# Kernel optimization log

Measured on AMD Instinct MI355X. Metric: run time of the kernel, lower is better.

Reference implementation:

```python
import jax, jax.numpy as jnp
import numpy as np

B = 4096
D = 2048
K = 8          # num_intention
H2 = 64        # fc2 out


def setup_inputs() -> dict:
    key = jax.random.key(0)
    ks = jax.random.split(key, 8)
    x = jax.random.normal(ks[0], (B, D), dtype=jnp.float32)
    # one-hot intention per sample
    idx = jax.random.randint(ks[1], (B,), 0, K)
    intention = jax.nn.one_hot(idx, K, dtype=jnp.float32)
    s1 = 1.0 / np.sqrt(D)
    s2 = 1.0 / np.sqrt(K)
    s3 = 1.0 / np.sqrt(D + H2)
    W1 = jax.random.uniform(ks[2], (D * K, D), jnp.float32, -s1, s1)
    b1 = jax.random.uniform(ks[3], (D * K,), jnp.float32, -s1, s1)
    W2 = jax.random.uniform(ks[4], (H2, K), jnp.float32, -s2, s2)
    b2 = jax.random.uniform(ks[5], (H2,), jnp.float32, -s2, s2)
    W3 = jax.random.uniform(ks[6], (1, D + H2), jnp.float32, -s3, s3)
    b3 = jax.random.uniform(ks[7], (1,), jnp.float32, -s3, s3)
    return {"x": x, "intention": intention, "W1": W1, "b1": b1,
            "W2": W2, "b2": b2, "W3": W3, "b3": b3}


def reference(x, intention, W1, b1, W2, b2, W3, b3):
    # fc2 on the one-hot intention -> [B, 64]
    y2 = intention @ W2.T + b2
    # fc1 densely computes all K branches (dropout treated as identity / eval mode)
    y1 = x @ W1.T + b1                      # [B, D*K]
    # mask = intention.repeat(1, 2048): branch axis is INNERMOST (interleaved)
    y1 = y1.reshape(B, D, K)                # [B, D, K]
    sel = jax.lax.stop_gradient(intention)  # mask is non-differentiable in torch
    y1 = jnp.einsum('bdk,bk->bd', y1, sel)  # gather active branch -> [B, D]
    y3 = jax.nn.relu(jnp.concatenate([y1, y2], axis=1))  # [B, D+64]
    y = y3 @ W3.T + b3                      # [B, 1]
    return y
```

## Files before the change

### kernel.cpp

```cpp
#include <hip/hip_runtime.h>
#include <hip/hip_bf16.h>
#include <stdint.h>

#define NB 4096
#define ND 2048
#define NK 8
#define NH 64

#define BM 128
#define BN 128
#define BK 32
#define MAX_ROWS 5120
#define MAX_TILES 40

#define CONV_BLOCKS  2048
#define KIDX_BLOCKS  (NB / 256)
#define PREP_GRID    (CONV_BLOCKS + KIDX_BLOCKS)
#define STRIPE 8388608

typedef __bf16 bf16;
typedef __bf16 bf16x8 __attribute__((ext_vector_type(8)));
typedef float floatx4 __attribute__((ext_vector_type(4)));

#define OFF_KIDX   0u
#define OFF_ORDER  16384u
#define OFF_META   40960u
#define OFF_CUR    41472u
#define OFF_C2S    41536u
#define OFF_CNTP   41600u
#define OFF_XC     65536u
#define OFF_WB     16842752u

__device__ inline void cvt16nt(const float* __restrict__ src, bf16* __restrict__ dst) {
    floatx4 a = __builtin_nontemporal_load((const floatx4*)src);
    floatx4 b = __builtin_nontemporal_load((const floatx4*)src + 1);
    floatx4 c = __builtin_nontemporal_load((const floatx4*)src + 2);
    floatx4 d = __builtin_nontemporal_load((const floatx4*)src + 3);
    bf16x8 v0, v1;
    v0[0] = (bf16)a[0]; v0[1] = (bf16)a[1]; v0[2] = (bf16)a[2]; v0[3] = (bf16)a[3];
    v0[4] = (bf16)b[0]; v0[5] = (bf16)b[1]; v0[6] = (bf16)b[2]; v0[7] = (bf16)b[3];
    v1[0] = (bf16)c[0]; v1[1] = (bf16)c[1]; v1[2] = (bf16)c[2]; v1[3] = (bf16)c[3];
    v1[4] = (bf16)d[0]; v1[5] = (bf16)d[1]; v1[6] = (bf16)d[2]; v1[7] = (bf16)d[3];
    *(bf16x8*)dst = v0;
    *((bf16x8*)dst + 1) = v1;
}

__global__ void __launch_bounds__(256)
prep_conv_kernel(const float* __restrict__ x,
                 const float* __restrict__ intention,
                 const float* __restrict__ W1,
                 int* __restrict__ kidx,
                 int* __restrict__ cntp,
                 bf16* __restrict__ xc,
                 bf16* __restrict__ Wb)
{
    const int blk = blockIdx.x;
    const int tid = threadIdx.x;

    if (blk < CONV_BLOCKS) {
        const size_t t16 = ((size_t)blk * 256 + tid) * 16;
#pragma unroll
        for (int i = 0; i < 4; i++)
            cvt16nt(W1 + (size_t)i * STRIPE + t16, Wb + (size_t)i * STRIPE + t16);
        cvt16nt(x + t16, xc + t16);
    } else {
        __shared__ int h[NK];
        const int hb = blk - CONV_BLOCKS;
        if (tid < NK) h[tid] = 0;
        __syncthreads();
        const int b = hb * 256 + tid;
        float4 a = *(const float4*)(intention + (size_t)b * NK);
        float4 c = *(const float4*)(intention + (size_t)b * NK + 4);
        int k = 0;
        if (a.y > 0.5f) k = 1;
        if (a.z > 0.5f) k = 2;
        if (a.w > 0.5f) k = 3;
        if (c.x > 0.5f) k = 4;
        if (c.y > 0.5f) k = 5;
        if (c.z > 0.5f) k = 6;
        if (c.w > 0.5f) k = 7;
        kidx[b] = k;
        atomicAdd(&h[k], 1);
        __syncthreads();
        if (tid < NK) cntp[hb * NK + tid] = h[tid];
    }
}

__global__ void __launch_bounds__(256)
meta_kernel(const int* __restrict__ cntp,
            const float* __restrict__ W2,
            const float* __restrict__ b2,
            const float* __restrict__ W3,
            const float* __restrict__ b3,
            int* __restrict__ meta,
            int* __restrict__ cursors,
            float* __restrict__ c2s)
{
    __shared__ int cnt[NK];
    const int tid = threadIdx.x;
    if (tid < NK) {
        int s = 0;
#pragma unroll
        for (int i = 0; i < KIDX_BLOCKS; i++) s += cntp[i * NK + tid];
        cnt[tid] = s;
    }
    if (tid >= 64 && tid < 128) {
        const int l = tid - 64;
        const int k = l & 7;
        const int hc = l >> 3;
        float s = 0.f;
#pragma unroll
        for (int j = 0; j < 8; j++) {
            int h = hc * 8 + j;
            float v = W2[h * NK + k] + b2[h];
            if (v > 0.f) s += v * W3[ND + h];
        }
        s += __shfl_xor(s, 8, 64);
        s += __shfl_xor(s, 16, 64);
        s += __shfl_xor(s, 32, 64);
        if (l < 8) c2s[k] = s + b3[0];
    }
    __syncthreads();
    if (tid == 0) {
        int running = 0, nt = 0;
        for (int k = 0; k < NK; k++) {
            cursors[k] = running;
            int ntile = (cnt[k] + BM - 1) / BM;
            for (int t = 0; t < ntile && nt < MAX_TILES; t++) {
                meta[1 + nt] = k;
                meta[1 + MAX_TILES + nt] = running + t * BM;
                nt++;
            }
            running += ntile * BM;
        }
        meta[0] = nt;
    }
}

__global__ void __launch_bounds__(256)
scatter_kernel(const int* __restrict__ kidx,
               int* __restrict__ cursors,
               const float* __restrict__ c2s,
               int* __restrict__ order,
               float* __restrict__ out)
{
    const int b = blockIdx.x * 256 + threadIdx.x;
    const int lane = threadIdx.x & 63;
    const int k = kidx[b] & 7;
    out[b] = c2s[k];

    const unsigned long long below = (lane == 63) ? ~0ull >> 1
                                   : ((1ull << lane) - 1);
    int pos = 0;
#pragma unroll
    for (int kk = 0; kk < NK; kk++) {
        unsigned long long m = __ballot(k == kk);
        if (m) {
            int leader = __ffsll((long long)m) - 1;
            int base = 0;
            if (lane == leader) base = atomicAdd(&cursors[kk], __popcll(m));
            base = __shfl(base, leader, 64);
            if (k == kk) pos = base + __popcll(m & below);
        }
    }
    if (pos >= 0 && pos < MAX_ROWS) order[pos] = b;
}

__global__ void __launch_bounds__(256)
gemm_kernel(const bf16* __restrict__ xc,
            const bf16* __restrict__ Wb,
            const int* __restrict__ order,
            const int* __restrict__ meta,
            const float* __restrict__ b1,
            const float* __restrict__ W3,
            float* __restrict__ out)
{
    int n_mt = meta[0];
    if (n_mt > MAX_TILES) n_mt = MAX_TILES;
    const int mt = blockIdx.y;
    if (mt >= n_mt) return;
    const int kbr = meta[1 + mt] & 7;
    int row0 = meta[1 + MAX_TILES + mt];
    if (row0 < 0) row0 = 0;
    if (row0 > MAX_ROWS - BM) row0 = MAX_ROWS - BM;
    const int col0 = blockIdx.x * BN;

    __shared__ bf16 As[BM * BK];
    __shared__ bf16 Bs[BN * BK];
    __shared__ int rowb[BM];

    const int tid = threadIdx.x;
    const int lane = tid & 63;
    const int wid = tid >> 6;
    const int wm = wid >> 1;
    const int wn = wid & 1;

    if (tid < BM) {
        int b = order[row0 + tid];
        rowb[tid] = (b >= 0 && b < NB) ? b : -1;
    }
    __syncthreads();

    const int srow = tid >> 2;
    const int scol = (tid & 3) * 8;
    const int ra0 = rowb[srow];
    const int ra1 = rowb[64 + srow];
    const bf16* pa0 = xc + (size_t)(ra0 < 0 ? 0 : ra0) * ND + scol;
    const bf16* pa1 = xc + (size_t)(ra1 < 0 ? 0 : ra1) * ND + scol;
    const bf16* pb0 = Wb + ((size_t)(col0 + srow) * NK + kbr) * ND + scol;
    const bf16* pb1 = pb0 + (size_t)64 * NK * ND;
    bf16* la0 = As + wid * 512;
    bf16* la1 = As + 2048 + wid * 512;
    bf16* lb0 = Bs + wid * 512;
    bf16* lb1 = Bs + 2048 + wid * 512;

    floatx4 zero = {0.f, 0.f, 0.f, 0.f};
    floatx4 acc[4][4];
#pragma unroll
    for (int i = 0; i < 4; i++)
#pragma unroll
        for (int j = 0; j < 4; j++) acc[i][j] = zero;

    const int qk = (lane >> 4) * 8;
    const int mrow = lane & 15;

    for (int kk = 0; kk < ND; kk += BK) {
        __builtin_amdgcn_global_load_lds(
            (const __attribute__((address_space(1))) void*)(pa0 + kk),
            (__attribute__((address_space(3))) void*)la0, 16, 0, 0);
        __builtin_amdgcn_global_load_lds(
            (const __attribute__((address_space(1))) void*)(pa1 + kk),
            (__attribute__((address_space(3))) void*)la1, 16, 0, 0);
        __builtin_amdgcn_global_load_lds(
            (const __attribute__((address_space(1))) void*)(pb0 + kk),
            (__attribute__((address_space(3))) void*)lb0, 16, 0, 0);
        __builtin_amdgcn_global_load_lds(
            (const __attribute__((address_space(1))) void*)(pb1 + kk),
            (__attribute__((address_space(3))) void*)lb1, 16, 0, 0);
        __syncthreads();

        bf16x8 af[4], bfv[4];
#pragma unroll
        for (int i = 0; i < 4; i++) {
            af[i]  = *(const bf16x8*)(As + (wm * 64 + i * 16 + mrow) * BK + qk);
            bfv[i] = *(const bf16x8*)(Bs + (wn * 64 + i * 16 + mrow) * BK + qk);
        }
#pragma unroll
        for (int i = 0; i < 4; i++)
#pragma unroll
            for (int j = 0; j < 4; j++)
                acc[i][j] = __builtin_amdgcn_mfma_f32_16x16x32_bf16(
                    af[i], bfv[j], acc[i][j], 0, 0, 0);
        __syncthreads();
    }

    const int colq = lane & 15;
    const int quad = lane >> 4;
    float bias[4], w3v[4];
#pragma unroll
    for (int j = 0; j < 4; j++) {
        int d = col0 + wn * 64 + j * 16 + colq;
        bias[j] = b1[d * NK + kbr];
        w3v[j] = W3[d];
    }
#pragma unroll
    for (int i = 0; i < 4; i++) {
#pragma unroll
        for (int r = 0; r < 4; r++) {
            float s = 0.f;
#pragma unroll
            for (int j = 0; j < 4; j++) {
                float v = acc[i][j][r] + bias[j];
                s += (v > 0.f) ? v * w3v[j] : 0.f;
            }
#pragma unroll
            for (int m = 1; m < 16; m <<= 1) s += __shfl_xor(s, m, 64);
            if (colq == 0) {
                int b = rowb[wm * 64 + i * 16 + quad * 4 + r];
                if (b >= 0) atomicAdd(out + b, s);
            }
        }
    }
}

extern "C" void kernel_launch(void* const* d_in, const int* in_sizes, int n_in,
                              void* d_out, int out_size, void* d_ws, size_t ws_size,
                              hipStream_t stream)
{
    const float* x         = (const float*)d_in[0];
    const float* intention = (const float*)d_in[1];
    const float* W1        = (const float*)d_in[2];
    const float* b1        = (const float*)d_in[3];
    const float* W2        = (const float*)d_in[4];
    const float* b2        = (const float*)d_in[5];
    const float* W3        = (const float*)d_in[6];
    const float* b3        = (const float*)d_in[7];
    float* out = (float*)d_out;

    char* ws = (char*)d_ws;
    int*   kidx    = (int*)(ws + OFF_KIDX);
    int*   order   = (int*)(ws + OFF_ORDER);
    int*   meta    = (int*)(ws + OFF_META);
    int*   cursors = (int*)(ws + OFF_CUR);
    float* c2s     = (float*)(ws + OFF_C2S);
    int*   cntp    = (int*)(ws + OFF_CNTP);
    bf16*  xc      = (bf16*)(ws + OFF_XC);
    bf16*  Wb      = (bf16*)(ws + OFF_WB);

    prep_conv_kernel<<<dim3(PREP_GRID), dim3(256), 0, stream>>>(
        x, intention, W1, kidx, cntp, xc, Wb);
    meta_kernel<<<dim3(1), dim3(256), 0, stream>>>(
        cntp, W2, b2, W3, b3, meta, cursors, c2s);
    scatter_kernel<<<dim3(NB / 256), dim3(256), 0, stream>>>(
        kidx, cursors, c2s, order, out);
    gemm_kernel<<<dim3(ND / BN, MAX_TILES), dim3(256), 0, stream>>>(
        xc, Wb, order, meta, b1, W3, out);
}
```

Measured before the change: 324.9 us.

## Triple-buffer LDS tiles with async global-to-LDS prefetch two steps ahead

Replaces the single-buffered K loop, which had two barriers per step, with a three-stage ring of LDS buffers. Global-to-LDS loads are issued two K-steps ahead, and explicit vmcnt waits plus one barrier per step let memory traffic overlap the MFMA work. In exchange the kernel uses three times the LDS for A and B tiles, which may reduce occupancy. It also relies on hand-written waitcnt counts being correct for the async loads.

```diff
diff --git a/kernel.cpp b/kernel.cpp
--- a/kernel.cpp
+++ b/kernel.cpp
@@ -12,6 +12,7 @@
 #define BK 32
 #define MAX_ROWS 5120
 #define MAX_TILES 40
+#define BUFSZ 4096
 
 #define CONV_BLOCKS  2048
 #define KIDX_BLOCKS  (NB / 256)
@@ -166,6 +167,41 @@
     if (pos >= 0 && pos < MAX_ROWS) order[pos] = b;
 }
 
+#define WAITBAR4 asm volatile("s_waitcnt vmcnt(4)\n\ts_barrier" ::: "memory")
+#define WAITBAR0 asm volatile("s_waitcnt vmcnt(0)\n\ts_barrier" ::: "memory")
+
+#define STAGE(aB, bB, kkel)                                                      \
+    do {                                                                         \
+        __builtin_amdgcn_global_load_lds(                                        \
+            (const __attribute__((address_space(1))) void*)(pa0 + (kkel)),       \
+            (__attribute__((address_space(3))) void*)((aB) + wid * 512), 16, 0, 0); \
+        __builtin_amdgcn_global_load_lds(                                        \
+            (const __attribute__((address_space(1))) void*)(pa1 + (kkel)),       \
+            (__attribute__((address_space(3))) void*)((aB) + 2048 + wid * 512), 16, 0, 0); \
+        __builtin_amdgcn_global_load_lds(                                        \
+            (const __attribute__((address_space(1))) void*)(pb0 + (kkel)),       \
+            (__attribute__((address_space(3))) void*)((bB) + wid * 512), 16, 0, 0); \
+        __builtin_amdgcn_global_load_lds(                                        \
+            (const __attribute__((address_space(1))) void*)(pb1 + (kkel)),       \
+            (__attribute__((address_space(3))) void*)((bB) + 2048 + wid * 512), 16, 0, 0); \
+    } while (0)
+
+#define COMPUTE(aB, bB)                                                          \
+    do {                                                                         \
+        bf16x8 af[4], bfv[4];                                                    \
+        _Pragma("unroll")                                                        \
+        for (int i = 0; i < 4; i++) {                                            \
+            af[i]  = *(const bf16x8*)((aB) + (wm * 64 + i * 16 + mrow) * BK + qk); \
+            bfv[i] = *(const bf16x8*)((bB) + (wn * 64 + i * 16 + mrow) * BK + qk); \
+        }                                                                        \
+        _Pragma("unroll")                                                        \
+        for (int i = 0; i < 4; i++)                                              \
+            _Pragma("unroll")                                                    \
+            for (int j = 0; j < 4; j++)                                          \
+                acc[i][j] = __builtin_amdgcn_mfma_f32_16x16x32_bf16(             \
+                    af[i], bfv[j], acc[i][j], 0, 0, 0);                          \
+    } while (0)
+
 __global__ void __launch_bounds__(256)
 gemm_kernel(const bf16* __restrict__ xc,
             const bf16* __restrict__ Wb,
@@ -185,8 +221,8 @@
     if (row0 > MAX_ROWS - BM) row0 = MAX_ROWS - BM;
     const int col0 = blockIdx.x * BN;
 
-    __shared__ bf16 As[BM * BK];
-    __shared__ bf16 Bs[BN * BK];
+    __shared__ bf16 As[3 * BUFSZ];
+    __shared__ bf16 Bs[3 * BUFSZ];
     __shared__ int rowb[BM];
 
     const int tid = threadIdx.x;
@@ -209,10 +245,6 @@
     const bf16* pa1 = xc + (size_t)(ra1 < 0 ? 0 : ra1) * ND + scol;
     const bf16* pb0 = Wb + ((size_t)(col0 + srow) * NK + kbr) * ND + scol;
     const bf16* pb1 = pb0 + (size_t)64 * NK * ND;
-    bf16* la0 = As + wid * 512;
-    bf16* la1 = As + 2048 + wid * 512;
-    bf16* lb0 = Bs + wid * 512;
-    bf16* lb1 = Bs + 2048 + wid * 512;
 
     floatx4 zero = {0.f, 0.f, 0.f, 0.f};
     floatx4 acc[4][4];
@@ -223,36 +255,24 @@
 
     const int qk = (lane >> 4) * 8;
     const int mrow = lane & 15;
-
-    for (int kk = 0; kk < ND; kk += BK) {
-        __builtin_amdgcn_global_load_lds(
-            (const __attribute__((address_space(1))) void*)(pa0 + kk),
-            (__attribute__((address_space(3))) void*)la0, 16, 0, 0);
-        __builtin_amdgcn_global_load_lds(
-            (const __attribute__((address_space(1))) void*)(pa1 + kk),
-            (__attribute__((address_space(3))) void*)la1, 16, 0, 0);
-        __builtin_amdgcn_global_load_lds(
-            (const __attribute__((address_space(1))) void*)(pb0 + kk),
-            (__attribute__((address_space(3))) void*)lb0, 16, 0, 0);
-        __builtin_amdgcn_global_load_lds(
-            (const __attribute__((address_space(1))) void*)(pb1 + kk),
-            (__attribute__((address_space(3))) void*)lb1, 16, 0, 0);
-        __syncthreads();
-
-        bf16x8 af[4], bfv[4];
-#pragma unroll
-        for (int i = 0; i < 4; i++) {
-            af[i]  = *(const bf16x8*)(As + (wm * 64 + i * 16 + mrow) * BK + qk);
-            bfv[i] = *(const bf16x8*)(Bs + (wn * 64 + i * 16 + mrow) * BK + qk);
-        }
-#pragma unroll
-        for (int i = 0; i < 4; i++)
-#pragma unroll
-            for (int j = 0; j < 4; j++)
-                acc[i][j] = __builtin_amdgcn_mfma_f32_16x16x32_bf16(
-                    af[i], bfv[j], acc[i][j], 0, 0, 0);
-        __syncthreads();
-    }
+    const int NSTEP = ND / BK;
+
+    STAGE(As, Bs, 0);
+    STAGE(As + BUFSZ, Bs + BUFSZ, BK);
+    int coff = 0;
+    int soff = 2 * BUFSZ;
+
+    for (int k = 0; k < NSTEP - 1; ++k) {
+        WAITBAR4;
+        if (k < NSTEP - 2) {
+            STAGE(As + soff, Bs + soff, (k + 2) * BK);
+            soff = (soff == 2 * BUFSZ) ? 0 : soff + BUFSZ;
+        }
+        COMPUTE(As + coff, Bs + coff);
+        coff = (coff == 2 * BUFSZ) ? 0 : coff + BUFSZ;
+    }
+    WAITBAR0;
+    COMPUTE(As + coff, Bs + coff);
 
     const int colq = lane & 15;
     const int quad = lane >> 4;
```

Result: no change. 331.1 us (+1.9%).

## Double GEMM K-tile to 64 and XOR-swizzle LDS layout to avoid bank conflicts

Applied to the files above, without the earlier changes.

Raises the K-step of the main grouped GEMM from 32 to 64, so each barrier pair covers two MFMA sub-steps and the number of K-loop iterations and syncs is halved. The global-to-LDS loads are reorganized so each wave loads 8-row groups with an XOR swizzle on the 16-byte chunk index, and the fragment reads apply the same swizzle. This is meant to reduce LDS bank conflicts on the 128-byte rows. LDS usage doubles and the loop stays single-buffered, so load latency is still not overlapped with compute.

```diff
diff --git a/kernel.cpp b/kernel.cpp
--- a/kernel.cpp
+++ b/kernel.cpp
@@ -9,7 +9,7 @@
 
 #define BM 128
 #define BN 128
-#define BK 32
+#define BK 64
 #define MAX_ROWS 5120
 #define MAX_TILES 40
 
@@ -201,18 +201,17 @@
     }
     __syncthreads();
 
-    const int srow = tid >> 2;
-    const int scol = (tid & 3) * 8;
-    const int ra0 = rowb[srow];
-    const int ra1 = rowb[64 + srow];
-    const bf16* pa0 = xc + (size_t)(ra0 < 0 ? 0 : ra0) * ND + scol;
-    const bf16* pa1 = xc + (size_t)(ra1 < 0 ? 0 : ra1) * ND + scol;
-    const bf16* pb0 = Wb + ((size_t)(col0 + srow) * NK + kbr) * ND + scol;
-    const bf16* pb1 = pb0 + (size_t)64 * NK * ND;
-    bf16* la0 = As + wid * 512;
-    bf16* la1 = As + 2048 + wid * 512;
-    bf16* lb0 = Bs + wid * 512;
-    bf16* lb1 = Bs + 2048 + wid * 512;
+    const int g8 = lane >> 3;
+    const int ssl = (lane & 7) ^ g8;
+    const bf16* pA[4];
+    const bf16* pB[4];
+#pragma unroll
+    for (int i = 0; i < 4; i++) {
+        int rl = wid * 32 + i * 8 + g8;
+        int ra = rowb[rl];
+        pA[i] = xc + (size_t)(ra < 0 ? 0 : ra) * ND + ssl * 8;
+        pB[i] = Wb + ((size_t)(col0 + rl) * NK + kbr) * ND + ssl * 8;
+    }
 
     floatx4 zero = {0.f, 0.f, 0.f, 0.f};
     floatx4 acc[4][4];
@@ -221,36 +220,41 @@
 #pragma unroll
         for (int j = 0; j < 4; j++) acc[i][j] = zero;
 
-    const int qk = (lane >> 4) * 8;
     const int mrow = lane & 15;
+    const int m7 = mrow & 7;
+    const int qs = lane >> 4;
+    const int sl0 = qs ^ m7;
 
     for (int kk = 0; kk < ND; kk += BK) {
-        __builtin_amdgcn_global_load_lds(
-            (const __attribute__((address_space(1))) void*)(pa0 + kk),
-            (__attribute__((address_space(3))) void*)la0, 16, 0, 0);
-        __builtin_amdgcn_global_load_lds(
-            (const __attribute__((address_space(1))) void*)(pa1 + kk),
-            (__attribute__((address_space(3))) void*)la1, 16, 0, 0);
-        __builtin_amdgcn_global_load_lds(
-            (const __attribute__((address_space(1))) void*)(pb0 + kk),
-            (__attribute__((address_space(3))) void*)lb0, 16, 0, 0);
-        __builtin_amdgcn_global_load_lds(
-            (const __attribute__((address_space(1))) void*)(pb1 + kk),
-            (__attribute__((address_space(3))) void*)lb1, 16, 0, 0);
+#pragma unroll
+        for (int i = 0; i < 4; i++) {
+            __builtin_amdgcn_global_load_lds(
+                (const __attribute__((address_space(1))) void*)(pA[i] + kk),
+                (__attribute__((address_space(3))) void*)(As + (wid * 32 + i * 8) * BK),
+                16, 0, 0);
+            __builtin_amdgcn_global_load_lds(
+                (const __attribute__((address_space(1))) void*)(pB[i] + kk),
+                (__attribute__((address_space(3))) void*)(Bs + (wid * 32 + i * 8) * BK),
+                16, 0, 0);
+        }
         __syncthreads();
 
-        bf16x8 af[4], bfv[4];
-#pragma unroll
-        for (int i = 0; i < 4; i++) {
-            af[i]  = *(const bf16x8*)(As + (wm * 64 + i * 16 + mrow) * BK + qk);
-            bfv[i] = *(const bf16x8*)(Bs + (wn * 64 + i * 16 + mrow) * BK + qk);
-        }
-#pragma unroll
-        for (int i = 0; i < 4; i++)
-#pragma unroll
-            for (int j = 0; j < 4; j++)
-                acc[i][j] = __builtin_amdgcn_mfma_f32_16x16x32_bf16(
-                    af[i], bfv[j], acc[i][j], 0, 0, 0);
+#pragma unroll
+        for (int h = 0; h < 2; h++) {
+            const int sh = (sl0 ^ (h << 2)) * 8;
+            bf16x8 af[4], bfv[4];
+#pragma unroll
+            for (int i = 0; i < 4; i++) {
+                af[i]  = *(const bf16x8*)(As + (wm * 64 + i * 16 + mrow) * BK + sh);
+                bfv[i] = *(const bf16x8*)(Bs + (wn * 64 + i * 16 + mrow) * BK + sh);
+            }
+#pragma unroll
+            for (int i = 0; i < 4; i++)
+#pragma unroll
+                for (int j = 0; j < 4; j++)
+                    acc[i][j] = __builtin_amdgcn_mfma_f32_16x16x32_bf16(
+                        af[i], bfv[j], acc[i][j], 0, 0, 0);
+        }
         __syncthreads();
     }
 
```

Result: slower. 336.8 us (+3.7%).

## Double-buffer LDS tiles to overlap global loads with MFMA compute

Applied to the files above, without the earlier changes.

Splits the shared A/B tiles into two buffers and prefetches the next K-slice via global_load_lds while the current slice is consumed by MFMAs. This halves the barriers per K step and hides global load latency behind compute. It doubles LDS usage, which may lower occupancy, and relies on the barrier after compute to make each prefetch visible.

```diff
diff --git a/kernel.cpp b/kernel.cpp
--- a/kernel.cpp
+++ b/kernel.cpp
@@ -166,6 +166,38 @@
     if (pos >= 0 && pos < MAX_ROWS) order[pos] = b;
 }
 
+#define STAGE(aB, bB, kkel)                                                         \
+    do {                                                                            \
+        __builtin_amdgcn_global_load_lds(                                           \
+            (const __attribute__((address_space(1))) void*)(pa0 + (kkel)),          \
+            (__attribute__((address_space(3))) void*)((aB) + wid * 512), 16, 0, 0); \
+        __builtin_amdgcn_global_load_lds(                                           \
+            (const __attribute__((address_space(1))) void*)(pa1 + (kkel)),          \
+            (__attribute__((address_space(3))) void*)((aB) + 2048 + wid * 512), 16, 0, 0); \
+        __builtin_amdgcn_global_load_lds(                                           \
+            (const __attribute__((address_space(1))) void*)(pb0 + (kkel)),          \
+            (__attribute__((address_space(3))) void*)((bB) + wid * 512), 16, 0, 0); \
+        __builtin_amdgcn_global_load_lds(                                           \
+            (const __attribute__((address_space(1))) void*)(pb1 + (kkel)),          \
+            (__attribute__((address_space(3))) void*)((bB) + 2048 + wid * 512), 16, 0, 0); \
+    } while (0)
+
+#define COMPUTE(aB, bB)                                                             \
+    do {                                                                            \
+        bf16x8 af[4], bfv[4];                                                       \
+        _Pragma("unroll")                                                           \
+        for (int i = 0; i < 4; i++) {                                               \
+            af[i]  = *(const bf16x8*)((aB) + (wm * 64 + i * 16 + mrow) * BK + qk);  \
+            bfv[i] = *(const bf16x8*)((bB) + (wn * 64 + i * 16 + mrow) * BK + qk);  \
+        }                                                                           \
+        _Pragma("unroll")                                                           \
+        for (int i = 0; i < 4; i++)                                                 \
+            _Pragma("unroll")                                                       \
+            for (int j = 0; j < 4; j++)                                             \
+                acc[i][j] = __builtin_amdgcn_mfma_f32_16x16x32_bf16(                \
+                    af[i], bfv[j], acc[i][j], 0, 0, 0);                             \
+    } while (0)
+
 __global__ void __launch_bounds__(256)
 gemm_kernel(const bf16* __restrict__ xc,
             const bf16* __restrict__ Wb,
@@ -185,8 +217,10 @@
     if (row0 > MAX_ROWS - BM) row0 = MAX_ROWS - BM;
     const int col0 = blockIdx.x * BN;
 
-    __shared__ bf16 As[BM * BK];
-    __shared__ bf16 Bs[BN * BK];
+    __shared__ bf16 As0[BM * BK];
+    __shared__ bf16 As1[BM * BK];
+    __shared__ bf16 Bs0[BN * BK];
+    __shared__ bf16 Bs1[BN * BK];
     __shared__ int rowb[BM];
 
     const int tid = threadIdx.x;
@@ -209,10 +243,6 @@
     const bf16* pa1 = xc + (size_t)(ra1 < 0 ? 0 : ra1) * ND + scol;
     const bf16* pb0 = Wb + ((size_t)(col0 + srow) * NK + kbr) * ND + scol;
     const bf16* pb1 = pb0 + (size_t)64 * NK * ND;
-    bf16* la0 = As + wid * 512;
-    bf16* la1 = As + 2048 + wid * 512;
-    bf16* lb0 = Bs + wid * 512;
-    bf16* lb1 = Bs + 2048 + wid * 512;
 
     floatx4 zero = {0.f, 0.f, 0.f, 0.f};
     floatx4 acc[4][4];
@@ -224,33 +254,15 @@
     const int qk = (lane >> 4) * 8;
     const int mrow = lane & 15;
 
-    for (int kk = 0; kk < ND; kk += BK) {
-        __builtin_amdgcn_global_load_lds(
-            (const __attribute__((address_space(1))) void*)(pa0 + kk),
-            (__attribute__((address_space(3))) void*)la0, 16, 0, 0);
-        __builtin_amdgcn_global_load_lds(
-            (const __attribute__((address_space(1))) void*)(pa1 + kk),
-            (__attribute__((address_space(3))) void*)la1, 16, 0, 0);
-        __builtin_amdgcn_global_load_lds(
-            (const __attribute__((address_space(1))) void*)(pb0 + kk),
-            (__attribute__((address_space(3))) void*)lb0, 16, 0, 0);
-        __builtin_amdgcn_global_load_lds(
-            (const __attribute__((address_space(1))) void*)(pb1 + kk),
-            (__attribute__((address_space(3))) void*)lb1, 16, 0, 0);
+    STAGE(As0, Bs0, 0);
+    __syncthreads();
+
+    for (int kk = 0; kk < ND; kk += 2 * BK) {
+        if (kk + BK < ND) STAGE(As1, Bs1, kk + BK);
+        COMPUTE(As0, Bs0);
         __syncthreads();
-
-        bf16x8 af[4], bfv[4];
-#pragma unroll
-        for (int i = 0; i < 4; i++) {
-            af[i]  = *(const bf16x8*)(As + (wm * 64 + i * 16 + mrow) * BK + qk);
-            bfv[i] = *(const bf16x8*)(Bs + (wn * 64 + i * 16 + mrow) * BK + qk);
-        }
-#pragma unroll
-        for (int i = 0; i < 4; i++)
-#pragma unroll
-            for (int j = 0; j < 4; j++)
-                acc[i][j] = __builtin_amdgcn_mfma_f32_16x16x32_bf16(
-                    af[i], bfv[j], acc[i][j], 0, 0, 0);
+        if (kk + 2 * BK < ND) STAGE(As0, Bs0, kk + 2 * BK);
+        COMPUTE(As1, Bs1);
         __syncthreads();
     }
 
```

Result: slower. 345.2 us (+6.2%).
